# Kernel optimization log

Measured on AMD Instinct MI355X. Metric: run time of the kernel, lower is better.

Reference implementation:

```python
import jax, jax.numpy as jnp
import numpy as np

DIM = 1024
HEADS = 16
HEAD_DIM = DIM // HEADS
BS, SQ, SK = 4, 2048, 2048


def setup_inputs() -> dict:
    key = jax.random.key(0)
    ks = jax.random.split(key, 12)
    s = 1.0 / np.sqrt(DIM)
    return {
        "x_q": jax.random.normal(ks[0], (BS, SQ, DIM), jnp.float32),
        "x_k": jax.random.normal(ks[1], (BS, SK, DIM), jnp.float32),
        "x_v": jax.random.normal(ks[2], (BS, SK, DIM), jnp.float32),
        "mask": jax.random.randint(ks[3], (BS, SQ, SK), 0, 2, jnp.int32),
        # torch nn.Linear weights: [out, in]; y = x @ W.T + b
        "wq": jax.random.uniform(ks[4], (DIM, DIM), jnp.float32, -s, s),
        "bq": jax.random.uniform(ks[5], (DIM,), jnp.float32, -s, s),
        "wk": jax.random.uniform(ks[6], (DIM, DIM), jnp.float32, -s, s),
        "bk": jax.random.uniform(ks[7], (DIM,), jnp.float32, -s, s),
        "wv": jax.random.uniform(ks[8], (DIM, DIM), jnp.float32, -s, s),
        "bv": jax.random.uniform(ks[9], (DIM,), jnp.float32, -s, s),
        "wo": jax.random.uniform(ks[10], (DIM, DIM), jnp.float32, -s, s),
        "bo": jax.random.uniform(ks[11], (DIM,), jnp.float32, -s, s),
    }


def reference(x_q, x_k, x_v, mask, wq, bq, wk, bk, wv, bv, wo, bo):
    bs, sq, dim = x_q.shape
    q = x_q @ wq.T + bq
    k = x_k @ wk.T + bk
    v = x_v @ wv.T + bv
    # [b, h, s, d]
    qh = q.reshape(bs, sq, HEADS, HEAD_DIM).transpose(0, 2, 1, 3)
    kh = k.reshape(bs, -1, HEADS, HEAD_DIM).transpose(0, 2, 1, 3)
    vh = v.reshape(bs, -1, HEADS, HEAD_DIM).transpose(0, 2, 1, 3)
    scale = 1.0 / np.sqrt(HEAD_DIM).astype(np.float32)
    s = jnp.einsum("bhqd,bhkd->bhqk", qh, kh) * scale
    # mask==0 positions set to -10000 across all heads
    s = jnp.where(mask[:, None, :, :] == 0, jnp.float32(-10000.0), s)
    p = jax.nn.softmax(s, axis=-1)
    z = jnp.einsum("bhqk,bhkd->bhqd", p, vh)
    z = z.transpose(0, 2, 1, 3).reshape(bs, sq, dim)
    return z @ wo.T + bo
```

## Files before the change

kernel.cpp:

```cpp
#include <hip/hip_runtime.h>

#define DEVINL __device__ __forceinline__

typedef _Float16 half8 __attribute__((ext_vector_type(8)));
typedef __fp16 fp16x2 __attribute__((ext_vector_type(2)));
typedef float f32x4 __attribute__((ext_vector_type(4)));
typedef float float4v __attribute__((ext_vector_type(4)));

static constexpr int kDIM = 1024;
static constexpr int kHEADS = 16;
static constexpr int kHD = 64;
static constexpr int kBS = 4;
static constexpr int kSQ = 2048;
static constexpr int kSK = 2048;
static constexpr int kMTOT = kBS * kSQ;

DEVINL void async_copy16(void* lds, const void* g) {
  __builtin_amdgcn_global_load_lds(
      (__attribute__((address_space(1))) unsigned int*)(g),
      (__attribute__((address_space(3))) unsigned int*)(lds), 16, 0, 0);
}

DEVINL unsigned pkrtz_u32(float a, float b) {
  fp16x2 h = __builtin_amdgcn_cvt_pkrtz(a, b);
  unsigned u;
  __builtin_memcpy(&u, &h, 4);
  return u;
}

__global__ void prep_kernel(const int* __restrict__ mask,
                            unsigned* __restrict__ bits,
                            const float* __restrict__ s0, const float* __restrict__ s1,
                            const float* __restrict__ s2, const float* __restrict__ s3,
                            _Float16* __restrict__ d0, _Float16* __restrict__ d1,
                            _Float16* __restrict__ d2, _Float16* __restrict__ d3) {
  int bid = blockIdx.x;
  if (bid < 2048) {
    int t = bid * 256 + threadIdx.x;
    const int4* p = (const int4*)(mask + (size_t)t * 32);
    unsigned w = 0;
#pragma unroll
    for (int j = 0; j < 8; ++j) {
      int4 v = p[j];
      w |= (v.x != 0 ? 1u : 0u) << (j * 4);
      w |= (v.y != 0 ? 1u : 0u) << (j * 4 + 1);
      w |= (v.z != 0 ? 1u : 0u) << (j * 4 + 2);
      w |= (v.w != 0 ? 1u : 0u) << (j * 4 + 3);
    }
    bits[t] = w;
  } else {
    int cb = bid - 2048;
    int which = cb >> 9;
    const float* s = which == 0 ? s0 : which == 1 ? s1 : which == 2 ? s2 : s3;
    _Float16* d = which == 0 ? d0 : which == 1 ? d1 : which == 2 ? d2 : d3;
    int j = ((cb & 511) * 256 + threadIdx.x) * 8;
    float4v a0 = *(const float4v*)(s + j);
    float4v a1 = *(const float4v*)(s + j + 4);
    half8 h;
    h[0] = (_Float16)a0[0]; h[1] = (_Float16)a0[1];
    h[2] = (_Float16)a0[2]; h[3] = (_Float16)a0[3];
    h[4] = (_Float16)a1[0]; h[5] = (_Float16)a1[1];
    h[6] = (_Float16)a1[2]; h[7] = (_Float16)a1[3];
    *(half8*)(d + j) = h;
  }
}

template <bool A_F32, bool OUT_F16>
DEVINL void gemm_body(const void* __restrict__ Aptr,
                      const _Float16* __restrict__ B,
                      const float* __restrict__ bias,
                      void* __restrict__ Cptr, int N, int K, int bid,
                      _Float16* As, _Float16* Bs) {
  const int tid = threadIdx.x;
  const int lane = tid & 63;
  const int w = tid >> 6;
  const int wr = w >> 1, wc = w & 1;
  const int bm0 = (bid & 63) << 7;
  const int bn0 = (bid >> 6) << 7;
  const int c16 = lane & 15;
  const int hi4 = lane >> 4;

  f32x4 acc[4][4] = {};

  for (int k0 = 0; k0 < K; k0 += 64) {
    __syncthreads();
    if (A_F32) {
      const float* A32 = (const float*)Aptr;
#pragma unroll
      for (int i = 0; i < 4; ++i) {
        int c = i * 256 + tid;
        int row = c >> 3, seg = c & 7;
        int gseg = seg ^ (row & 7);
        const float* src = A32 + (size_t)(bm0 + row) * K + k0 + gseg * 8;
        float4v a0 = *(const float4v*)src;
        float4v a1 = *(const float4v*)(src + 4);
        half8 h;
        h[0] = (_Float16)a0[0]; h[1] = (_Float16)a0[1];
        h[2] = (_Float16)a0[2]; h[3] = (_Float16)a0[3];
        h[4] = (_Float16)a1[0]; h[5] = (_Float16)a1[1];
        h[6] = (_Float16)a1[2]; h[7] = (_Float16)a1[3];
        *(half8*)((char*)As + c * 16) = h;
      }
    } else {
      const _Float16* A16 = (const _Float16*)Aptr;
#pragma unroll
      for (int i = 0; i < 4; ++i) {
        int c = i * 256 + tid;
        int row = c >> 3, seg = c & 7;
        int gseg = seg ^ (row & 7);
        async_copy16((char*)As + i * 4096 + w * 1024,
                     A16 + (size_t)(bm0 + row) * K + k0 + gseg * 8);
      }
    }
#pragma unroll
    for (int i = 0; i < 4; ++i) {
      int c = i * 256 + tid;
      int row = c >> 3, seg = c & 7;
      int gseg = seg ^ (row & 7);
      async_copy16((char*)Bs + i * 4096 + w * 1024,
                   B + (size_t)(bn0 + row) * K + k0 + gseg * 8);
    }
    __syncthreads();
#pragma unroll
    for (int kf = 0; kf < 2; ++kf) {
      half8 af[4], bf[4];
#pragma unroll
      for (int m = 0; m < 4; ++m) {
        int row = wr * 64 + m * 16 + c16;
        int off = row * 128 + (((kf * 4 + hi4) << 4) ^ ((row & 7) << 4));
        af[m] = *(const half8*)((const char*)As + off);
      }
#pragma unroll
      for (int n = 0; n < 4; ++n) {
        int row = wc * 64 + n * 16 + c16;
        int off = row * 128 + (((kf * 4 + hi4) << 4) ^ ((row & 7) << 4));
        bf[n] = *(const half8*)((const char*)Bs + off);
      }
#pragma unroll
      for (int m = 0; m < 4; ++m)
#pragma unroll
        for (int n = 0; n < 4; ++n)
          acc[m][n] =
              __builtin_amdgcn_mfma_f32_16x16x32_f16(af[m], bf[n], acc[m][n], 0, 0, 0);
    }
  }
#pragma unroll
  for (int n = 0; n < 4; ++n) {
    int col = bn0 + wc * 64 + n * 16 + c16;
    float bv = bias[col];
#pragma unroll
    for (int m = 0; m < 4; ++m) {
      int row0 = bm0 + wr * 64 + m * 16 + (hi4 << 2);
#pragma unroll
      for (int r = 0; r < 4; ++r) {
        float v = acc[m][n][r] + bv;
        if (OUT_F16)
          ((_Float16*)Cptr)[(size_t)(row0 + r) * N + col] = (_Float16)v;
        else
          ((float*)Cptr)[(size_t)(row0 + r) * N + col] = v;
      }
    }
  }
}

__launch_bounds__(256, 2)
__global__ void gemm_qkv_kernel(const float* __restrict__ xq,
                                const float* __restrict__ xk,
                                const float* __restrict__ xv,
                                const _Float16* __restrict__ Wq,
                                const _Float16* __restrict__ Wk,
                                const _Float16* __restrict__ Wv,
                                const float* __restrict__ bq,
                                const float* __restrict__ bk,
                                const float* __restrict__ bv,
                                _Float16* __restrict__ Q16,
                                _Float16* __restrict__ K16,
                                _Float16* __restrict__ V16) {
  __shared__ __align__(16) _Float16 As[128 * 64];
  __shared__ __align__(16) _Float16 Bs[128 * 64];
  int which = blockIdx.x >> 9;
  int bid = blockIdx.x & 511;
  const float* A = which == 0 ? xq : which == 1 ? xk : xv;
  const _Float16* B = which == 0 ? Wq : which == 1 ? Wk : Wv;
  const float* bias = which == 0 ? bq : which == 1 ? bk : bv;
  _Float16* C = which == 0 ? Q16 : which == 1 ? K16 : V16;
  gemm_body<true, true>(A, B, bias, C, kDIM, kDIM, bid, As, Bs);
}

__launch_bounds__(256, 2)
__global__ void gemm_o_kernel(const _Float16* __restrict__ Z16,
                              const _Float16* __restrict__ Wo,
                              const float* __restrict__ bo,
                              float* __restrict__ out) {
  __shared__ __align__(16) _Float16 As[128 * 64];
  __shared__ __align__(16) _Float16 Bs[128 * 64];
  gemm_body<false, false>(Z16, Wo, bo, out, kDIM, kDIM, blockIdx.x, As, Bs);
}

__global__ void transpose_v_kernel(const _Float16* __restrict__ V,
                                   _Float16* __restrict__ Vt) {
  __shared__ _Float16 tile[64][72];
  int bh = blockIdx.y;
  int b = bh >> 4, h = bh & 15;
  int s0 = blockIdx.x * 64;
  int tid = threadIdx.x;
  {
    int s = tid >> 2, dseg = tid & 3;
    const half8* src =
        (const half8*)(V + (size_t)(b * kSK + s0 + s) * kDIM + h * 64 + dseg * 16);
    half8 v0 = src[0], v1 = src[1];
#pragma unroll
    for (int j = 0; j < 8; ++j) {
      tile[s][dseg * 16 + j] = v0[j];
      tile[s][dseg * 16 + 8 + j] = v1[j];
    }
  }
  __syncthreads();
  {
    int d = tid >> 2, sseg = tid & 3;
    half8 o0, o1;
#pragma unroll
    for (int j = 0; j < 8; ++j) {
      o0[j] = tile[sseg * 16 + j][d];
      o1[j] = tile[sseg * 16 + 8 + j][d];
    }
    half8* dst = (half8*)(Vt + ((size_t)(bh * 64 + d)) * kSK + s0 + sseg * 16);
    dst[0] = o0;
    dst[1] = o1;
  }
}

__launch_bounds__(256, 3)
__global__ void attn_kernel(const _Float16* __restrict__ Q,
                            const _Float16* __restrict__ K,
                            const _Float16* __restrict__ Vt,
                            const unsigned* __restrict__ maskbits,
                            _Float16* __restrict__ Z) {
  __shared__ __align__(16) char smem[32768 + 128 * 72 * 2];
  _Float16* Ps = (_Float16*)(smem + 32768);
  const int tid = threadIdx.x, lane = tid & 63, w = tid >> 6;
  const int bid = blockIdx.x;
  const int hb = bid & 63;
  const int b = hb >> 4, h = hb & 15;
  const int qt0 = (bid >> 6) * 128;
  const int c16 = lane & 15;
  const int hi4 = lane >> 4;
  const int row4 = hi4 << 2;
  const unsigned* mb = maskbits + (size_t)b * kSQ * (kSK / 32);

#pragma unroll
  for (int i = 0; i < 4; ++i) {
    int c = i * 256 + tid;
    int row = c >> 3, seg = c & 7;
    int gseg = seg ^ (row & 7);
    async_copy16(smem + i * 4096 + w * 1024,
                 Q + (size_t)(b * kSQ + qt0 + row) * kDIM + h * 64 + gseg * 8);
  }
  __syncthreads();
  half8 qf[2][2];
#pragma unroll
  for (int m = 0; m < 2; ++m)
#pragma unroll
    for (int kf = 0; kf < 2; ++kf) {
      int row = w * 32 + m * 16 + c16;
      int off = row * 128 + (((kf * 4 + hi4) << 4) ^ ((row & 7) << 4));
      qf[m][kf] = *(const half8*)(smem + off);
      qf[m][kf] *= (_Float16)0.18033688f;
    }
  __syncthreads();

  auto stage_kv = [&](int bufoff, int ktt) {
#pragma unroll
    for (int i = 0; i < 2; ++i) {
      int c = i * 256 + tid;
      int row = c >> 3, seg = c & 7;
      int gseg = seg ^ (row & 7);
      async_copy16(smem + bufoff + i * 4096 + w * 1024,
                   K + (size_t)(b * kSK + ktt + row) * kDIM + h * 64 + gseg * 8);
    }
#pragma unroll
    for (int i = 0; i < 2; ++i) {
      int c = i * 256 + tid;
      int row = c >> 3, seg = c & 7;
      int gseg = seg ^ (row & 7);
      async_copy16(smem + bufoff + 8192 + i * 4096 + w * 1024,
                   Vt + (size_t)((b * kHEADS + h) * kHD + row) * kSK + ktt + gseg * 8);
    }
  };

  unsigned long long mq_cur[2], mq_nxt[2];
  stage_kv(0, 0);
#pragma unroll
  for (int m2 = 0; m2 < 2; ++m2) {
    int q = qt0 + w * 32 + m2 * 16 + c16;
    mq_cur[m2] = *(const unsigned long long*)(mb + (size_t)q * (kSK / 32));
  }
  asm volatile("s_waitcnt vmcnt(0)" ::: "memory");
  __builtin_amdgcn_s_barrier();
  asm volatile("" ::: "memory");

  f32x4 zacc[2][4] = {};
  f32x4 lacc[2] = {};
  half8 ones8;
#pragma unroll
  for (int j = 0; j < 8; ++j) ones8[j] = (_Float16)1.0f;

  int cur = 0;
  for (int kt = 0; kt < kSK; kt += 64) {
    if (kt + 64 < kSK) {
      stage_kv((cur ^ 1) * 16384, kt + 64);
#pragma unroll
      for (int m2 = 0; m2 < 2; ++m2) {
        int q = qt0 + w * 32 + m2 * 16 + c16;
        mq_nxt[m2] = *(const unsigned long long*)(mb + (size_t)q * (kSK / 32) +
                                                  ((kt + 64) >> 5));
      }
    }
    const char* bufK = smem + cur * 16384;
    const char* bufV = bufK + 8192;

    f32x4 s[2][4] = {};
    __builtin_amdgcn_s_setprio(1);
#pragma unroll
    for (int kf = 0; kf < 2; ++kf)
#pragma unroll
      for (int n = 0; n < 4; ++n) {
        int key = n * 16 + c16;
        half8 kb = *(const half8*)(bufK + key * 128 +
                                   (((kf * 4 + hi4) << 4) ^ ((key & 7) << 4)));
        s[0][n] = __builtin_amdgcn_mfma_f32_16x16x32_f16(kb, qf[0][kf], s[0][n], 0, 0, 0);
        s[1][n] = __builtin_amdgcn_mfma_f32_16x16x32_f16(kb, qf[1][kf], s[1][n], 0, 0, 0);
      }
    __builtin_amdgcn_s_setprio(0);

#pragma unroll
    for (int m2 = 0; m2 < 2; ++m2) {
      unsigned lo = (unsigned)(mq_cur[m2] >> (hi4 * 4));
      unsigned hh = (unsigned)(mq_cur[m2] >> (hi4 * 4 + 32));
      int q_local = w * 32 + m2 * 16 + c16;
#pragma unroll
      for (int n = 0; n < 4; ++n) {
        unsigned sel = (n < 2) ? lo : hh;
        const int base = (n & 1) * 16;
        float p[4];
#pragma unroll
        for (int r = 0; r < 4; ++r) {
          float pv = __builtin_exp2f(s[m2][n][r]);
          int msk = __builtin_amdgcn_sbfe((int)sel, base + r, 1);
          pv = __uint_as_float(__float_as_uint(pv) & (unsigned)msk);
          p[r] = pv;
        }
        uint2 pw = {pkrtz_u32(p[0], p[1]), pkrtz_u32(p[2], p[3])};
        *(uint2*)((char*)Ps + q_local * 144 + n * 32 + hi4 * 8) = pw;
      }
    }

    __builtin_amdgcn_s_setprio(1);
#pragma unroll
    for (int kf2 = 0; kf2 < 2; ++kf2) {
      half8 vb[4];
#pragma unroll
      for (int df = 0; df < 4; ++df) {
        int d = df * 16 + c16;
        vb[df] = *(const half8*)(bufV + d * 128 +
                                 (((kf2 * 4 + hi4) << 4) ^ ((d & 7) << 4)));
      }
#pragma unroll
      for (int m2 = 0; m2 < 2; ++m2) {
        int q_local = w * 32 + m2 * 16 + c16;
        half8 pa = *(const half8*)((char*)Ps + q_local * 144 + (kf2 * 4 + hi4) * 16);
        lacc[m2] = __builtin_amdgcn_mfma_f32_16x16x32_f16(pa, ones8, lacc[m2], 0, 0, 0);
#pragma unroll
        for (int df = 0; df < 4; ++df)
          zacc[m2][df] =
              __builtin_amdgcn_mfma_f32_16x16x32_f16(pa, vb[df], zacc[m2][df], 0, 0, 0);
      }
    }
    __builtin_amdgcn_s_setprio(0);

    asm volatile("s_waitcnt vmcnt(0)" ::: "memory");
    __builtin_amdgcn_s_barrier();
    asm volatile("" ::: "memory");
    mq_cur[0] = mq_nxt[0];
    mq_cur[1] = mq_nxt[1];
    cur ^= 1;
  }

#pragma unroll
  for (int m2 = 0; m2 < 2; ++m2)
#pragma unroll
    for (int r = 0; r < 4; ++r) {
      float inv = 1.0f / lacc[m2][r];
      int q = qt0 + w * 32 + m2 * 16 + row4 + r;
#pragma unroll
      for (int df = 0; df < 4; ++df) {
        int d = df * 16 + c16;
        Z[(size_t)(b * kSQ + q) * kDIM + h * 64 + d] =
            (_Float16)(zacc[m2][df][r] * inv);
      }
    }
}

extern "C" void kernel_launch(void* const* d_in, const int* in_sizes, int n_in,
                              void* d_out, int out_size, void* d_ws,
                              size_t ws_size, hipStream_t stream) {
  const float* x_q = (const float*)d_in[0];
  const float* x_k = (const float*)d_in[1];
  const float* x_v = (const float*)d_in[2];
  const int* mask = (const int*)d_in[3];
  const float* wq = (const float*)d_in[4];
  const float* bq = (const float*)d_in[5];
  const float* wk = (const float*)d_in[6];
  const float* bk = (const float*)d_in[7];
  const float* wv = (const float*)d_in[8];
  const float* bv = (const float*)d_in[9];
  const float* wo = (const float*)d_in[10];
  const float* bo = (const float*)d_in[11];

  const size_t W_ELEMS = (size_t)1024 * 1024;
  const size_t T_ELEMS = (size_t)kMTOT * kDIM;
  const size_t NEED = (4 * W_ELEMS + 5 * T_ELEMS) * 2 + (size_t)kBS * kSQ * (kSK / 32) * 4;
  if (ws_size < NEED) return;

  char* ws = (char*)d_ws;
  _Float16* Wq16 = (_Float16*)ws;
  _Float16* Wk16 = Wq16 + W_ELEMS;
  _Float16* Wv16 = Wk16 + W_ELEMS;
  _Float16* Wo16 = Wv16 + W_ELEMS;
  _Float16* Q16 = Wo16 + W_ELEMS;
  _Float16* K16 = Q16 + T_ELEMS;
  _Float16* V16 = K16 + T_ELEMS;
  _Float16* Vt16 = V16 + T_ELEMS;
  _Float16* Z16 = Vt16 + T_ELEMS;
  unsigned* mbits = (unsigned*)(Z16 + T_ELEMS);

  prep_kernel<<<4096, 256, 0, stream>>>(mask, mbits, wq, wk, wv, wo,
                                        Wq16, Wk16, Wv16, Wo16);

  gemm_qkv_kernel<<<1536, 256, 0, stream>>>(x_q, x_k, x_v, Wq16, Wk16, Wv16,
                                            bq, bk, bv, Q16, K16, V16);

  transpose_v_kernel<<<dim3(32, 64), 256, 0, stream>>>(V16, Vt16);

  attn_kernel<<<1024, 256, 0, stream>>>(Q16, K16, Vt16, mbits, Z16);

  gemm_o_kernel<<<512, 256, 0, stream>>>(Z16, Wo16, bo, (float*)d_out);
}
```

Measured before the change: 257.7 us.

## Keep softmax probabilities in registers and feed PV MFMA directly, dropping LDS staging

The attention kernel no longer writes exponentiated probabilities to shared memory and reads them back. It uses the S accumulator layout directly as the B operand of 16x16x16 MFMAs, with V loaded in a matching half4 layout and the output transposed so Z rows are written as packed 8-byte stores. The freed LDS and precomputed offsets allow raising launch bounds to 4 blocks per CU. The trade-off is twice as many smaller MFMA instructions, plus register pressure under the tighter occupancy bound.

```diff
diff --git a/kernel.cpp b/kernel.cpp
--- a/kernel.cpp
+++ b/kernel.cpp
@@ -3,6 +3,7 @@
 #define DEVINL __device__ __forceinline__
 
 typedef _Float16 half8 __attribute__((ext_vector_type(8)));
+typedef _Float16 half4 __attribute__((ext_vector_type(4)));
 typedef __fp16 fp16x2 __attribute__((ext_vector_type(2)));
 typedef float f32x4 __attribute__((ext_vector_type(4)));
 typedef float float4v __attribute__((ext_vector_type(4)));
@@ -230,14 +231,13 @@
   }
 }
 
-__launch_bounds__(256, 3)
+__launch_bounds__(256, 4)
 __global__ void attn_kernel(const _Float16* __restrict__ Q,
                             const _Float16* __restrict__ K,
                             const _Float16* __restrict__ Vt,
                             const unsigned* __restrict__ maskbits,
                             _Float16* __restrict__ Z) {
-  __shared__ __align__(16) char smem[32768 + 128 * 72 * 2];
-  _Float16* Ps = (_Float16*)(smem + 32768);
+  __shared__ __align__(16) char smem[32768];
   const int tid = threadIdx.x, lane = tid & 63, w = tid >> 6;
   const int bid = blockIdx.x;
   const int hb = bid & 63;
@@ -245,7 +245,6 @@
   const int qt0 = (bid >> 6) * 128;
   const int c16 = lane & 15;
   const int hi4 = lane >> 4;
-  const int row4 = hi4 << 2;
   const unsigned* mb = maskbits + (size_t)b * kSQ * (kSK / 32);
 
 #pragma unroll
@@ -269,6 +268,24 @@
     }
   __syncthreads();
 
+  int kb_off[2][4];
+#pragma unroll
+  for (int kf = 0; kf < 2; ++kf)
+#pragma unroll
+    for (int n = 0; n < 4; ++n) {
+      int key = n * 16 + c16;
+      kb_off[kf][n] = key * 128 + (((kf * 4 + hi4) << 4) ^ ((key & 7) << 4));
+    }
+  int va_off[4][4];
+#pragma unroll
+  for (int n = 0; n < 4; ++n)
+#pragma unroll
+    for (int df = 0; df < 4; ++df) {
+      int d = df * 16 + c16;
+      int t = n * 2 + (hi4 >> 1);
+      va_off[n][df] = d * 128 + (((t ^ (d & 7)) << 4) | ((hi4 & 1) * 8));
+    }
+
   auto stage_kv = [&](int bufoff, int ktt) {
 #pragma unroll
     for (int i = 0; i < 2; ++i) {
@@ -301,9 +318,9 @@
 
   f32x4 zacc[2][4] = {};
   f32x4 lacc[2] = {};
-  half8 ones8;
-#pragma unroll
-  for (int j = 0; j < 8; ++j) ones8[j] = (_Float16)1.0f;
+  half4 ones4;
+#pragma unroll
+  for (int j = 0; j < 4; ++j) ones4[j] = (_Float16)1.0f;
 
   int cur = 0;
   for (int kt = 0; kt < kSK; kt += 64) {
@@ -325,23 +342,24 @@
     for (int kf = 0; kf < 2; ++kf)
 #pragma unroll
       for (int n = 0; n < 4; ++n) {
-        int key = n * 16 + c16;
-        half8 kb = *(const half8*)(bufK + key * 128 +
-                                   (((kf * 4 + hi4) << 4) ^ ((key & 7) << 4)));
+        half8 kb = *(const half8*)(bufK + kb_off[kf][n]);
         s[0][n] = __builtin_amdgcn_mfma_f32_16x16x32_f16(kb, qf[0][kf], s[0][n], 0, 0, 0);
         s[1][n] = __builtin_amdgcn_mfma_f32_16x16x32_f16(kb, qf[1][kf], s[1][n], 0, 0, 0);
       }
     __builtin_amdgcn_s_setprio(0);
 
-#pragma unroll
-    for (int m2 = 0; m2 < 2; ++m2) {
-      unsigned lo = (unsigned)(mq_cur[m2] >> (hi4 * 4));
-      unsigned hh = (unsigned)(mq_cur[m2] >> (hi4 * 4 + 32));
-      int q_local = w * 32 + m2 * 16 + c16;
-#pragma unroll
-      for (int n = 0; n < 4; ++n) {
-        unsigned sel = (n < 2) ? lo : hh;
-        const int base = (n & 1) * 16;
+    const unsigned lo0 = (unsigned)(mq_cur[0] >> (hi4 * 4));
+    const unsigned hh0 = (unsigned)(mq_cur[0] >> (hi4 * 4 + 32));
+    const unsigned lo1 = (unsigned)(mq_cur[1] >> (hi4 * 4));
+    const unsigned hh1 = (unsigned)(mq_cur[1] >> (hi4 * 4 + 32));
+
+#pragma unroll
+    for (int n = 0; n < 4; ++n) {
+      const int base = (n & 1) * 16;
+      half4 pb[2];
+#pragma unroll
+      for (int m2 = 0; m2 < 2; ++m2) {
+        unsigned sel = (n < 2) ? (m2 ? lo1 : lo0) : (m2 ? hh1 : hh0);
         float p[4];
 #pragma unroll
         for (int r = 0; r < 4; ++r) {
@@ -350,33 +368,24 @@
           pv = __uint_as_float(__float_as_uint(pv) & (unsigned)msk);
           p[r] = pv;
         }
-        uint2 pw = {pkrtz_u32(p[0], p[1]), pkrtz_u32(p[2], p[3])};
-        *(uint2*)((char*)Ps + q_local * 144 + n * 32 + hi4 * 8) = pw;
-      }
-    }
-
-    __builtin_amdgcn_s_setprio(1);
-#pragma unroll
-    for (int kf2 = 0; kf2 < 2; ++kf2) {
-      half8 vb[4];
-#pragma unroll
-      for (int df = 0; df < 4; ++df) {
-        int d = df * 16 + c16;
-        vb[df] = *(const half8*)(bufV + d * 128 +
-                                 (((kf2 * 4 + hi4) << 4) ^ ((d & 7) << 4)));
-      }
+        uint2 pu = {pkrtz_u32(p[0], p[1]), pkrtz_u32(p[2], p[3])};
+        __builtin_memcpy(&pb[m2], &pu, 8);
+      }
+      half4 va[4];
+#pragma unroll
+      for (int df = 0; df < 4; ++df)
+        va[df] = *(const half4*)(bufV + va_off[n][df]);
+      __builtin_amdgcn_s_setprio(1);
 #pragma unroll
       for (int m2 = 0; m2 < 2; ++m2) {
-        int q_local = w * 32 + m2 * 16 + c16;
-        half8 pa = *(const half8*)((char*)Ps + q_local * 144 + (kf2 * 4 + hi4) * 16);
-        lacc[m2] = __builtin_amdgcn_mfma_f32_16x16x32_f16(pa, ones8, lacc[m2], 0, 0, 0);
+        lacc[m2] = __builtin_amdgcn_mfma_f32_16x16x16f16(ones4, pb[m2], lacc[m2], 0, 0, 0);
 #pragma unroll
         for (int df = 0; df < 4; ++df)
-          zacc[m2][df] =
-              __builtin_amdgcn_mfma_f32_16x16x32_f16(pa, vb[df], zacc[m2][df], 0, 0, 0);
-      }
-    }
-    __builtin_amdgcn_s_setprio(0);
+          zacc[m2][df] = __builtin_amdgcn_mfma_f32_16x16x16f16(va[df], pb[m2],
+                                                               zacc[m2][df], 0, 0, 0);
+      }
+      __builtin_amdgcn_s_setprio(0);
+    }
 
     asm volatile("s_waitcnt vmcnt(0)" ::: "memory");
     __builtin_amdgcn_s_barrier();
@@ -387,18 +396,16 @@
   }
 
 #pragma unroll
-  for (int m2 = 0; m2 < 2; ++m2)
-#pragma unroll
-    for (int r = 0; r < 4; ++r) {
-      float inv = 1.0f / lacc[m2][r];
-      int q = qt0 + w * 32 + m2 * 16 + row4 + r;
-#pragma unroll
-      for (int df = 0; df < 4; ++df) {
-        int d = df * 16 + c16;
-        Z[(size_t)(b * kSQ + q) * kDIM + h * 64 + d] =
-            (_Float16)(zacc[m2][df][r] * inv);
-      }
-    }
+  for (int m2 = 0; m2 < 2; ++m2) {
+    float inv = 1.0f / lacc[m2][0];
+    int q = qt0 + w * 32 + m2 * 16 + c16;
+#pragma unroll
+    for (int df = 0; df < 4; ++df) {
+      uint2 zw = {pkrtz_u32(zacc[m2][df][0] * inv, zacc[m2][df][1] * inv),
+                  pkrtz_u32(zacc[m2][df][2] * inv, zacc[m2][df][3] * inv)};
+      *(uint2*)(Z + (size_t)(b * kSQ + q) * kDIM + h * 64 + df * 16 + hi4 * 4) = zw;
+    }
+  }
 }
 
 extern "C" void kernel_launch(void* const* d_in, const int* in_sizes, int n_in,
```

New measurement: 288.9 us. 12.1% more time.
